# Optimization experiments

Measured on AMD Instinct MI355X. Metric: run time of the kernel, lower is better.

Reference implementation:

```python
import jax, jax.numpy as jnp
import numpy as np

# Model dims (match init_kwargs)
N_HEADS = 32
N_KV_HEADS = 8
DIM = 4096
HEAD_DIM = DIM // N_HEADS  # 128
N_REP = N_HEADS // N_KV_HEADS  # 4
MAX_SEQ_LEN = 2048
THETA = 10000.0


def precompute_freqs(dim, end, theta=THETA):
    inv = 1.0 / (theta ** (jnp.arange(0, dim, 2, dtype=jnp.float32) / dim))  # [dim/2]
    t = jnp.arange(end, dtype=jnp.float32)
    f = jnp.outer(t, inv)  # [end, dim/2]
    return jnp.cos(f), jnp.sin(f)


def apply_rope(x, cos, sin):
    # x: [b, s, h, d]; cos/sin: [s, d/2]. Pairs (x[...,2i], x[...,2i+1]) form complex numbers.
    xr = x[..., 0::2]
    xi = x[..., 1::2]
    c = cos[None, :, None, :]
    s = sin[None, :, None, :]
    out_r = xr * c - xi * s
    out_i = xr * s + xi * c
    return jnp.stack([out_r, out_i], axis=-1).reshape(x.shape)


def setup_inputs() -> dict:
    key = jax.random.key(0)
    ks = jax.random.split(key, 5)
    B, S = 4, 1024
    x = jax.random.normal(ks[0], (B, S, DIM), dtype=jnp.float32)
    wq = jax.random.normal(ks[1], (DIM, N_HEADS * HEAD_DIM), dtype=jnp.float32) * 0.02
    wk = jax.random.normal(ks[2], (DIM, N_KV_HEADS * HEAD_DIM), dtype=jnp.float32) * 0.02
    wv = jax.random.normal(ks[3], (DIM, N_KV_HEADS * HEAD_DIM), dtype=jnp.float32) * 0.02
    wo = jax.random.normal(ks[4], (N_HEADS * HEAD_DIM, DIM), dtype=jnp.float32) * 0.02
    # causal mask, additive: 0 on/below diagonal, -1e9 above
    mask = jnp.where(jnp.tril(jnp.ones((S, S), dtype=bool)), 0.0, -1e9).astype(jnp.float32)[None, None]
    return {"x": x, "wq": wq, "wk": wk, "wv": wv, "wo": wo, "mask": mask, "start_pos": 0}


def reference(x, wq, wk, wv, wo, mask, start_pos):
    B, S, _ = x.shape
    # QKV projections
    xq = (x @ wq).reshape(B, S, N_HEADS, HEAD_DIM)
    xk = (x @ wk).reshape(B, S, N_KV_HEADS, HEAD_DIM)
    xv = (x @ wv).reshape(B, S, N_KV_HEADS, HEAD_DIM)
    # RoPE on q, k at positions [start_pos, start_pos+S)
    cos, sin = precompute_freqs(HEAD_DIM, MAX_SEQ_LEN * 2)
    cos_s = jax.lax.dynamic_slice_in_dim(cos, start_pos, S, 0)
    sin_s = jax.lax.dynamic_slice_in_dim(sin, start_pos, S, 0)
    xq = apply_rope(xq, cos_s, sin_s)
    xk = apply_rope(xk, cos_s, sin_s)
    # KV-cache scatter-update (cache starts zeroed), then read prefix
    cache_k = jnp.zeros((B, MAX_SEQ_LEN, N_KV_HEADS, HEAD_DIM), dtype=x.dtype)
    cache_v = jnp.zeros_like(cache_k)
    cache_k = jax.lax.dynamic_update_slice(cache_k, xk, (0, start_pos, 0, 0))
    cache_v = jax.lax.dynamic_update_slice(cache_v, xv, (0, start_pos, 0, 0))
    kv_len = start_pos + S
    keys = cache_k[:, :kv_len]    # [b, kv_len, n_kv, d]
    values = cache_v[:, :kv_len]
    # GQA without materializing repeated KV: split q heads into (kv_group, rep)
    q = xq.reshape(B, S, N_KV_HEADS, N_REP, HEAD_DIM)
    scale = 1.0 / jnp.sqrt(jnp.float32(HEAD_DIM)).astype(x.dtype)
    scores = jnp.einsum('bsgrd,btgd->bgrst', q, keys) * scale  # [b, g, r, s, t]
    scores = scores + mask.reshape(1, 1, 1, S, kv_len)
    probs = jax.nn.softmax(scores, axis=-1)
    out = jnp.einsum('bgrst,btgd->bsgrd', probs, values)  # [b, s, g, r, d]
    out = out.reshape(B, S, N_HEADS * HEAD_DIM)
    return out @ wo
```

## Files before the change

kernel.cpp:

```cpp
#include <hip/hip_runtime.h>
#include <hip/hip_bf16.h>
#include <stdint.h>

typedef __bf16 bf16raw;
typedef __attribute__((ext_vector_type(8))) __bf16 bf16x8;
typedef __attribute__((ext_vector_type(4))) float f32x4;

#define DIMD 4096
#define NHEAD 32
#define NKVH 8
#define HD 128
#define SEQ 1024
#define NB 4
#define NTOK 4096
#define NQKV 6144

__device__ __forceinline__ void gload_lds16(const void* gsrc, void* ldst) {
  __builtin_amdgcn_global_load_lds(
      (const __attribute__((address_space(1))) void*)gsrc,
      (__attribute__((address_space(3))) void*)ldst, 16, 0, 0);
}

__global__ void cast_f32_bf16_kernel(const float* __restrict__ src,
                                     __hip_bfloat16* __restrict__ dst, int n) {
  int i = (blockIdx.x * 256 + threadIdx.x) * 8;
  if (i >= n) return;
  f32x4 a = *(const f32x4*)(src + i);
  f32x4 b = *(const f32x4*)(src + i + 4);
  union { bf16x8 v; __hip_bfloat16 e[8]; } o;
#pragma unroll
  for (int j = 0; j < 4; ++j) {
    o.e[j] = __float2bfloat16(a[j]);
    o.e[4 + j] = __float2bfloat16(b[j]);
  }
  *(bf16x8*)(dst + i) = o.v;
}

__global__ void transpose_qkv_kernel(const float* __restrict__ wq,
                                     const float* __restrict__ wk,
                                     const float* __restrict__ wv,
                                     __hip_bfloat16* __restrict__ dst) {
  __shared__ float tile[32][33];
  int n0 = blockIdx.x * 32;
  int k0 = blockIdx.y * 32;
  const float* src;
  int scol, nsw;
  if (n0 < 4096) { src = wq; scol = n0; nsw = 4096; }
  else if (n0 < 5120) { src = wk; scol = n0 - 4096; nsw = 1024; }
  else { src = wv; scol = n0 - 5120; nsw = 1024; }
  int tx = threadIdx.x, ty = threadIdx.y;
#pragma unroll
  for (int i = 0; i < 4; ++i)
    tile[ty + 8 * i][tx] = src[(size_t)(k0 + ty + 8 * i) * nsw + scol + tx];
  __syncthreads();
  union { ushort4 u; __hip_bfloat16 e[4]; } pk;
#pragma unroll
  for (int jj = 0; jj < 4; ++jj)
    pk.e[jj] = __float2bfloat16(tile[ty * 4 + jj][tx]);
  *(ushort4*)(dst + (size_t)(n0 + tx) * 4096 + k0 + ty * 4) = pk.u;
}

__global__ void transpose_wo_kernel(const float* __restrict__ src,
                                    __hip_bfloat16* __restrict__ dst) {
  __shared__ float tile[32][33];
  int n0 = blockIdx.x * 32, k0 = blockIdx.y * 32;
  int tx = threadIdx.x, ty = threadIdx.y;
#pragma unroll
  for (int i = 0; i < 4; ++i)
    tile[ty + 8 * i][tx] = src[(size_t)(k0 + ty + 8 * i) * 4096 + n0 + tx];
  __syncthreads();
  union { ushort4 u; __hip_bfloat16 e[4]; } pk;
#pragma unroll
  for (int jj = 0; jj < 4; ++jj)
    pk.e[jj] = __float2bfloat16(tile[ty * 4 + jj][tx]);
  *(ushort4*)(dst + (size_t)(n0 + tx) * 4096 + k0 + ty * 4) = pk.u;
}

__global__ void rope_table_kernel(float* __restrict__ cosb, float* __restrict__ sinb) {
  int idx = blockIdx.x * 256 + threadIdx.x;
  int s = idx >> 6, j = idx & 63;
  float inv = 1.0f / powf(10000.0f, (float)(2 * j) * (1.0f / 128.0f));
  float ang = (float)s * inv;
  cosb[idx] = cosf(ang);
  sinb[idx] = sinf(ang);
}


#define LGSB()                                       \
  asm volatile("s_waitcnt lgkmcnt(0)" ::: "memory"); \
  __builtin_amdgcn_sched_barrier(0)

#define QM_LO(AFR, MB)                                                     \
  _Pragma("unroll") for (int mf2 = 0; mf2 < 4; ++mf2)                      \
  _Pragma("unroll") for (int nf2 = 0; nf2 < 2; ++nf2)                      \
  _Pragma("unroll") for (int kk2 = 0; kk2 < 2; ++kk2)                      \
      acc[(MB) + mf2][nf2] = __builtin_amdgcn_mfma_f32_16x16x32_bf16(      \
          AFR[mf2 * 2 + kk2], bql[nf2 * 2 + kk2], acc[(MB) + mf2][nf2], 0, 0, 0)

#define QM_HI(AFR, MB)                                                     \
  _Pragma("unroll") for (int mf2 = 0; mf2 < 4; ++mf2)                      \
  _Pragma("unroll") for (int nf2 = 0; nf2 < NF - 2; ++nf2)                 \
  _Pragma("unroll") for (int kk2 = 0; kk2 < 2; ++kk2)                      \
      acc[(MB) + mf2][2 + nf2] = __builtin_amdgcn_mfma_f32_16x16x32_bf16(  \
          AFR[mf2 * 2 + kk2], bqh[nf2 * 2 + kk2], acc[(MB) + mf2][2 + nf2], 0, 0, 0)

#define TILE4(BUF, ST1, ST2, ST3, ST4, VM)                        \
  {                                                               \
    ST1;                                                          \
    _Pragma("unroll") for (int mf = 0; mf < 4; ++mf)              \
    _Pragma("unroll") for (int kk = 0; kk < 2; ++kk)              \
        alo[mf * 2 + kk] = ldsA(BUF, mf, kk);                     \
    _Pragma("unroll") for (int nf = 0; nf < 2; ++nf)              \
    _Pragma("unroll") for (int kk = 0; kk < 2; ++kk)              \
        bql[nf * 2 + kk] = ldsB(BUF, nf, kk);                     \
    LGSB();                                                       \
    __builtin_amdgcn_s_setprio(1);                                \
    QM_LO(alo, 0);                                                \
    __builtin_amdgcn_s_setprio(0);                                \
    _Pragma("unroll") for (int mf = 0; mf < 4; ++mf)              \
    _Pragma("unroll") for (int kk = 0; kk < 2; ++kk)              \
        ahi[mf * 2 + kk] = ldsA(BUF, mf + 4, kk);                 \
    ST2;                                                          \
    LGSB();                                                       \
    __builtin_amdgcn_s_setprio(1);                                \
    QM_LO(ahi, 4);                                                \
    __builtin_amdgcn_s_setprio(0);                                \
    _Pragma("unroll") for (int nf = 0; nf < NF - 2; ++nf)         \
    _Pragma("unroll") for (int kk = 0; kk < 2; ++kk)              \
        bqh[nf * 2 + kk] = ldsB(BUF, nf + 2, kk);                 \
    LGSB();                                                       \
    __builtin_amdgcn_s_setprio(1);                                \
    QM_HI(alo, 0);                                                \
    __builtin_amdgcn_s_setprio(0);                                \
    __builtin_amdgcn_s_barrier();   \
    ST3;                                                          \
    ST4;                                                          \
    __builtin_amdgcn_s_setprio(1);                                \
    QM_HI(ahi, 4);                                                \
    __builtin_amdgcn_s_setprio(0);                                \
    VM;                                                           \
    __builtin_amdgcn_s_barrier();   \
  }

template <typename OutT, bool ROPE, int BN, int XM, int XN, int PM, int PN>
__global__ __launch_bounds__(512, 2) void gemm256_kernel(
    const __hip_bfloat16* __restrict__ A, const __hip_bfloat16* __restrict__ BT,
    OutT* __restrict__ C, int M, int N, int K,
    const float* __restrict__ cosb, const float* __restrict__ sinb,
    __hip_bfloat16* __restrict__ vtc) {
  constexpr int NF = BN / 64;
  constexpr int BROWS_W = BN / 8;
  constexpr int BQ = BN / 4;
  constexpr int BUFS = 32768 + BN * 128;
  __shared__ __align__(16) char lds_[2 * BUFS];
  const int tid = threadIdx.x;
  const int w = tid >> 6, l = tid & 63;
  const int lr = l & 15, lk = l >> 4;
  const int wm = w >> 2, wn = w & 3;

  const int bid = blockIdx.x;
  const int x = bid & 7, idx = bid >> 3;
  const int xr = x % XM, xc = x / XM;
  const int m0 = (xr * PM + idx / PN) << 8;
  const int n0 = (xc * PN + idx % PN) * BN;

  const size_t Kb = (size_t)K * 2;
  const char* Ab = (const char*)A + (size_t)m0 * Kb;
  const char* Bb = (const char*)BT + (size_t)n0 * Kb;
  const int srcb = ((l & 7) ^ (l >> 3)) * 16;
  const int crow = l >> 3;

  auto stageA = [&](int buf, int half, int kt) {
#pragma unroll
    for (int j = 0; j < 2; ++j) {
      int row = half * 128 + (w * 2 + j) * 8 + crow;
      gload_lds16(Ab + (size_t)row * Kb + (size_t)kt * 128 + srcb,
                  lds_ + buf * BUFS + half * 16384 + (w * 2 + j) * 1024);
    }
  };
  auto stageBlo = [&](int buf, int kt) {
#pragma unroll
    for (int j = 0; j < 2; ++j) {
      int row = w * BROWS_W + j * 8 + crow;
      gload_lds16(Bb + (size_t)row * Kb + (size_t)kt * 128 + srcb,
                  lds_ + buf * BUFS + 32768 + (w * BROWS_W + j * 8) * 128);
    }
  };
  auto stageBhi = [&](int buf, int kt) {
#pragma unroll
    for (int j = 2; j < NF; ++j) {
      int row = w * BROWS_W + j * 8 + crow;
      gload_lds16(Bb + (size_t)row * Kb + (size_t)kt * 128 + srcb,
                  lds_ + buf * BUFS + 32768 + (w * BROWS_W + j * 8) * 128);
    }
  };
  auto ldsA = [&](int buf, int mf, int kk) {
    int rih = mf * 16 + lr;
    int cb = (kk * 64 + lk * 16) ^ ((lr & 7) << 4);
    return *(const bf16x8*)(lds_ + buf * BUFS + wm * 16384 + rih * 128 + cb);
  };
  auto ldsB = [&](int buf, int nf, int kk) {
    int row = wn * BQ + nf * 16 + lr;
    int cb = (kk * 64 + lk * 16) ^ ((lr & 7) << 4);
    return *(const bf16x8*)(lds_ + buf * BUFS + 32768 + row * 128 + cb);
  };

  f32x4 acc[8][NF] = {};
  bf16x8 alo[8], ahi[8], bql[4], bqh[4];

  stageA(0, 0, 0);
  stageA(0, 1, 0);
  stageBlo(0, 0);
  stageBhi(0, 0);
  stageA(1, 0, 1);
  stageA(1, 1, 1);
  asm volatile("s_waitcnt vmcnt(4)" ::: "memory");
  __builtin_amdgcn_s_barrier();

  const int NT = K >> 6;
  for (int E = 0; E < NT - 2; E += 2) {
    TILE4(0, stageBlo(1, E + 1), stageBhi(1, E + 1),
          stageA(0, 0, E + 2), stageA(0, 1, E + 2),
          asm volatile("s_waitcnt vmcnt(4)" ::: "memory"));
    TILE4(1, stageBlo(0, E + 2), stageBhi(0, E + 2),
          stageA(1, 0, E + 3), stageA(1, 1, E + 3),
          asm volatile("s_waitcnt vmcnt(4)" ::: "memory"));
  }
  TILE4(0, stageBlo(1, NT - 1), stageBhi(1, NT - 1), (void)0, (void)0,
        asm volatile("s_waitcnt vmcnt(0)" ::: "memory"));
  TILE4(1, (void)0, (void)0, (void)0, (void)0, (void)0);

#pragma unroll
  for (int mf = 0; mf < 8; ++mf) {
    int row = m0 + wm * 128 + mf * 16 + lk * 4;
#pragma unroll
    for (int nf = 0; nf < NF; ++nf) {
      int colb = n0 + wn * BQ + nf * 16;
      f32x4 v = acc[mf][nf];
      if constexpr (ROPE) {
        if (colb < 5120) {
          int d = (colb & 127) + lr;
          int jj = d >> 1;
          bool even = (d & 1) == 0;
#pragma unroll
          for (int j = 0; j < 4; ++j) {
            float p = __shfl_xor(v[j], 1);
            int s = (row + j) & (SEQ - 1);
            float c = cosb[s * 64 + jj];
            float sn = sinb[s * 64 + jj];
            v[j] = even ? (v[j] * c - p * sn) : (p * sn + v[j] * c);
          }
        } else {
          int col = colb + lr;
          int d = col & 127;
          int hk = (col >> 7) & 7;
          int b = row >> 10;
          int s = row & (SEQ - 1);
          union { uint64_t u; __hip_bfloat16 e[4]; } pk;
#pragma unroll
          for (int j = 0; j < 4; ++j) pk.e[j] = __float2bfloat16(v[j]);
          size_t off = ((size_t)((b * 8 + hk) * 16 + (s >> 6)) * 128 + d) * 64 +
                       (s & 63);
          *(uint64_t*)(vtc + off) = pk.u;
          continue;
        }
      }
#pragma unroll
      for (int j = 0; j < 4; ++j) {
        size_t off = (size_t)(row + j) * N + colb + lr;
        if constexpr (sizeof(OutT) == 2)
          C[off] = __float2bfloat16(v[j]);
        else
          C[off] = v[j];
      }
    }
  }
}

__global__ __launch_bounds__(512, 2) void attn_kernel(
    const __hip_bfloat16* __restrict__ qkv,
    const __hip_bfloat16* __restrict__ vtc,
    __hip_bfloat16* __restrict__ out) {
  __shared__ __align__(16) char Ks[2][16384];
  __shared__ __align__(16) char Vs[2][16384];
  __shared__ __align__(16) char Ps[8][4096];

  const int tid = threadIdx.x;
  const int w = tid >> 6, l = tid & 63;
  const int lr = l & 15, lk = l >> 4;
  const int bx = blockIdx.x;
  const int p = bx >> 5;
  const int bh = bx & 31;
  const int b = bh >> 3;
  const int hk = bh & 7;
  const int h = hk * 4 + (w & 3);
  const int qh = w >> 2;

  const char* KgB = (const char*)qkv +
                    ((size_t)(b * SEQ) * NQKV + DIMD + hk * HD) * 2;
  const char* VgB = (const char*)vtc + (size_t)(b * NKVH + hk) * (16 * 16384);
  char* Pw = &Ps[w][0];

  const float cs = 0.12752039889171495f;
  const float ebias = 11.541560327111707f;

  auto stageK = [&](int buf, int kvb) {
#pragma unroll
    for (int j = 0; j < 2; ++j) {
      int i2 = w * 2 + j;
      int row = i2 * 4 + (l >> 4);
      int si = ((l & 15) * 16) ^ ((row & 7) << 4);
      gload_lds16(KgB + (size_t)(kvb + row) * (NQKV * 2) + si,
                  &Ks[buf][i2 * 1024]);
    }
  };
  auto stageV = [&](int buf, int t) {
#pragma unroll
    for (int j = 0; j < 2; ++j) {
      int i2 = w * 2 + j;
      int row = i2 * 8 + (l >> 3);
      int si = ((l & 7) * 16) ^ ((row & 7) << 4);
      gload_lds16(VgB + (size_t)t * 16384 + row * 128 + si,
                  &Vs[buf][i2 * 1024]);
    }
  };

  for (int qsel = 0; qsel < 2; ++qsel) {
    const int qtile = qsel ? (15 - p) : p;
    const int qbaseW = qtile * 64 + qh * 32;
    const int nkv = qtile + 1;

    bf16x8 aq[8];
#pragma unroll
    for (int qg = 0; qg < 2; ++qg) {
      const __hip_bfloat16* Qp =
          qkv + (size_t)(b * SEQ + qbaseW + qg * 16 + lr) * NQKV + h * HD + lk * 8;
#pragma unroll
      for (int ks = 0; ks < 4; ++ks) aq[qg * 4 + ks] = *(const bf16x8*)(Qp + ks * 32);
    }

    f32x4 O[16] = {};
    float lsum[8] = {0.f, 0.f, 0.f, 0.f, 0.f, 0.f, 0.f, 0.f};

    stageK(0, 0);
    stageV(0, 0);
    asm volatile("s_waitcnt vmcnt(0)" ::: "memory");
    __syncthreads();

    for (int t = 0; t < nkv; ++t) {
      const int cur = t & 1;
      if (t + 1 < nkv) {
        stageK(cur ^ 1, (t + 1) * 64);
        stageV(cur ^ 1, t + 1);
      }
      const int kvb = t * 64;

      f32x4 st[8] = {};
      __builtin_amdgcn_s_setprio(1);
#pragma unroll
      for (int nt = 0; nt < 4; ++nt) {
        int row = nt * 16 + lr;
        const char* kr = &Ks[cur][row * 256];
        int sw = (row & 7) << 4;
        bf16x8 bk[4];
#pragma unroll
        for (int ks = 0; ks < 4; ++ks)
          bk[ks] = *(const bf16x8*)(kr + ((ks * 64 + lk * 16) ^ sw));
#pragma unroll
        for (int qg = 0; qg < 2; ++qg)
#pragma unroll
          for (int ks = 0; ks < 4; ++ks)
            st[qg * 4 + nt] = __builtin_amdgcn_mfma_f32_16x16x32_bf16(
                aq[qg * 4 + ks], bk[ks], st[qg * 4 + nt], 0, 0, 0);
      }
      __builtin_amdgcn_s_setprio(0);

#pragma unroll
      for (int qg = 0; qg < 2; ++qg) {
        const bool needmask = (kvb + 63 > qbaseW + qg * 16);
#pragma unroll
        for (int j = 0; j < 4; ++j) {
          int qrow = qbaseW + qg * 16 + lk * 4 + j;
          int prow = lk * 4 + j;
          int sw = (prow & 7) << 4;
#pragma unroll
          for (int nt = 0; nt < 4; ++nt) {
            float pv = exp2f(fmaf(st[qg * 4 + nt][j], cs, -ebias));
            if (needmask && (kvb + nt * 16 + lr > qrow)) pv = 0.f;
            lsum[qg * 4 + j] += pv;
            *(__hip_bfloat16*)(Pw + qg * 2048 + prow * 128 +
                               (((nt * 16 + lr) * 2) ^ sw)) = __float2bfloat16(pv);
          }
        }
      }

      asm volatile("s_waitcnt lgkmcnt(0)" ::: "memory");
      __builtin_amdgcn_sched_barrier(0);

      __builtin_amdgcn_s_setprio(1);
#pragma unroll
      for (int ks = 0; ks < 2; ++ks) {
        bf16x8 ap[2];
#pragma unroll
        for (int qg = 0; qg < 2; ++qg)
          ap[qg] = *(const bf16x8*)(Pw + qg * 2048 + lr * 128 +
                                    ((ks * 64 + lk * 16) ^ ((lr & 7) << 4)));
#pragma unroll
        for (int dt = 0; dt < 8; ++dt) {
          int row = dt * 16 + lr;
          bf16x8 bv = *(const bf16x8*)(&Vs[cur][row * 128 +
                                               ((ks * 64 + lk * 16) ^ ((row & 7) << 4))]);
#pragma unroll
          for (int qg = 0; qg < 2; ++qg)
            O[qg * 8 + dt] = __builtin_amdgcn_mfma_f32_16x16x32_bf16(
                ap[qg], bv, O[qg * 8 + dt], 0, 0, 0);
        }
      }
      __builtin_amdgcn_s_setprio(0);

      __syncthreads();
    }

#pragma unroll
    for (int qg = 0; qg < 2; ++qg) {
#pragma unroll
      for (int j = 0; j < 4; ++j) {
        float rs = lsum[qg * 4 + j];
        rs += __shfl_xor(rs, 1);
        rs += __shfl_xor(rs, 2);
        rs += __shfl_xor(rs, 4);
        rs += __shfl_xor(rs, 8);
        float inv = 1.0f / rs;
        __hip_bfloat16* orow =
            out + (size_t)(b * SEQ + qbaseW + qg * 16 + lk * 4 + j) * DIMD + h * HD;
#pragma unroll
        for (int dt = 0; dt < 8; ++dt)
          orow[dt * 16 + lr] = __float2bfloat16(O[qg * 8 + dt][j] * inv);
      }
    }
  }
}

extern "C" void kernel_launch(void* const* d_in, const int* in_sizes, int n_in,
                              void* d_out, int out_size, void* d_ws, size_t ws_size,
                              hipStream_t stream) {
  const float* x = (const float*)d_in[0];
  const float* wq = (const float*)d_in[1];
  const float* wk = (const float*)d_in[2];
  const float* wv = (const float*)d_in[3];
  const float* wo = (const float*)d_in[4];
  float* out = (float*)d_out;

  char* ws = (char*)d_ws;
  const size_t MB = 1024 * 1024;
  __hip_bfloat16* xb = (__hip_bfloat16*)(ws);
  __hip_bfloat16* wqkvt = (__hip_bfloat16*)(ws + 32 * MB);
  __hip_bfloat16* wot = (__hip_bfloat16*)(ws + 80 * MB);
  __hip_bfloat16* qkv = (__hip_bfloat16*)(ws + 112 * MB);
  __hip_bfloat16* vtc = (__hip_bfloat16*)(ws + 160 * MB);
  float* cosb = (float*)(ws + 168 * MB);
  float* sinb = cosb + SEQ * 64;

  cast_f32_bf16_kernel<<<NTOK * DIMD / 8 / 256, 256, 0, stream>>>(x, xb, NTOK * DIMD);
  transpose_qkv_kernel<<<dim3(192, 128), dim3(32, 8), 0, stream>>>(wq, wk, wv, wqkvt);
  transpose_wo_kernel<<<dim3(128, 128), dim3(32, 8), 0, stream>>>(wo, wot);
  rope_table_kernel<<<SEQ * 64 / 256, 256, 0, stream>>>(cosb, sinb);
  gemm256_kernel<__hip_bfloat16, true, 192, 2, 4, 8, 8><<<dim3(512), 512, 0, stream>>>(
      xb, wqkvt, qkv, NTOK, NQKV, DIMD, cosb, sinb, vtc);
  attn_kernel<<<dim3(256), 512, 0, stream>>>(qkv, vtc, xb);
  gemm256_kernel<float, false, 256, 4, 2, 4, 8><<<dim3(256), 512, 0, stream>>>(
      xb, wot, out, NTOK, DIMD, DIMD, nullptr, nullptr, nullptr);
}
```

Measured before the change: 444.2 us.

## Halve attention query tile per block and double grid for higher occupancy

The attention kernel now gives each warp one 16-row query group instead of two, so each block covers 32 query rows and the grid doubles to 512 blocks. Causal load balancing still pairs tile p with tile 31-p. Accumulator and P-buffer sizes halve, and the launch bounds ask for 4 blocks per CU instead of 2, to improve occupancy and latency hiding. In exchange, each K/V tile staged in LDS is reused by half as many query rows, which roughly doubles K/V load traffic.

After: 443.5 us. Within noise of the previous version (-0.1%).

```diff
diff --git a/kernel.cpp b/kernel.cpp
--- a/kernel.cpp
+++ b/kernel.cpp
@@ -277,13 +277,13 @@
   }
 }
 
-__global__ __launch_bounds__(512, 2) void attn_kernel(
+__global__ __launch_bounds__(512, 4) void attn_kernel(
     const __hip_bfloat16* __restrict__ qkv,
     const __hip_bfloat16* __restrict__ vtc,
     __hip_bfloat16* __restrict__ out) {
   __shared__ __align__(16) char Ks[2][16384];
   __shared__ __align__(16) char Vs[2][16384];
-  __shared__ __align__(16) char Ps[8][4096];
+  __shared__ __align__(16) char Ps[8][2048];
 
   const int tid = threadIdx.x;
   const int w = tid >> 6, l = tid & 63;
@@ -326,21 +326,20 @@
   };
 
   for (int qsel = 0; qsel < 2; ++qsel) {
-    const int qtile = qsel ? (15 - p) : p;
-    const int qbaseW = qtile * 64 + qh * 32;
-    const int nkv = qtile + 1;
-
-    bf16x8 aq[8];
-#pragma unroll
-    for (int qg = 0; qg < 2; ++qg) {
+    const int qtile = qsel ? (31 - p) : p;
+    const int qbase = qtile * 32 + qh * 16;
+    const int nkv = (qtile >> 1) + 1;
+
+    bf16x8 aq[4];
+    {
       const __hip_bfloat16* Qp =
-          qkv + (size_t)(b * SEQ + qbaseW + qg * 16 + lr) * NQKV + h * HD + lk * 8;
-#pragma unroll
-      for (int ks = 0; ks < 4; ++ks) aq[qg * 4 + ks] = *(const bf16x8*)(Qp + ks * 32);
-    }
-
-    f32x4 O[16] = {};
-    float lsum[8] = {0.f, 0.f, 0.f, 0.f, 0.f, 0.f, 0.f, 0.f};
+          qkv + (size_t)(b * SEQ + qbase + lr) * NQKV + h * HD + lk * 8;
+#pragma unroll
+      for (int ks = 0; ks < 4; ++ks) aq[ks] = *(const bf16x8*)(Qp + ks * 32);
+    }
+
+    f32x4 O[8] = {};
+    float lsum[4] = {0.f, 0.f, 0.f, 0.f};
 
     stageK(0, 0);
     stageV(0, 0);
@@ -355,42 +354,34 @@
       }
       const int kvb = t * 64;
 
-      f32x4 st[8] = {};
+      f32x4 st[4] = {};
       __builtin_amdgcn_s_setprio(1);
 #pragma unroll
       for (int nt = 0; nt < 4; ++nt) {
         int row = nt * 16 + lr;
         const char* kr = &Ks[cur][row * 256];
         int sw = (row & 7) << 4;
-        bf16x8 bk[4];
-#pragma unroll
-        for (int ks = 0; ks < 4; ++ks)
-          bk[ks] = *(const bf16x8*)(kr + ((ks * 64 + lk * 16) ^ sw));
-#pragma unroll
-        for (int qg = 0; qg < 2; ++qg)
-#pragma unroll
-          for (int ks = 0; ks < 4; ++ks)
-            st[qg * 4 + nt] = __builtin_amdgcn_mfma_f32_16x16x32_bf16(
-                aq[qg * 4 + ks], bk[ks], st[qg * 4 + nt], 0, 0, 0);
+#pragma unroll
+        for (int ks = 0; ks < 4; ++ks) {
+          bf16x8 bk = *(const bf16x8*)(kr + ((ks * 64 + lk * 16) ^ sw));
+          st[nt] = __builtin_amdgcn_mfma_f32_16x16x32_bf16(aq[ks], bk, st[nt], 0, 0, 0);
+        }
       }
       __builtin_amdgcn_s_setprio(0);
 
-#pragma unroll
-      for (int qg = 0; qg < 2; ++qg) {
-        const bool needmask = (kvb + 63 > qbaseW + qg * 16);
-#pragma unroll
-        for (int j = 0; j < 4; ++j) {
-          int qrow = qbaseW + qg * 16 + lk * 4 + j;
-          int prow = lk * 4 + j;
-          int sw = (prow & 7) << 4;
-#pragma unroll
-          for (int nt = 0; nt < 4; ++nt) {
-            float pv = exp2f(fmaf(st[qg * 4 + nt][j], cs, -ebias));
-            if (needmask && (kvb + nt * 16 + lr > qrow)) pv = 0.f;
-            lsum[qg * 4 + j] += pv;
-            *(__hip_bfloat16*)(Pw + qg * 2048 + prow * 128 +
-                               (((nt * 16 + lr) * 2) ^ sw)) = __float2bfloat16(pv);
-          }
+      const bool needmask = (kvb + 63 > qbase);
+#pragma unroll
+      for (int j = 0; j < 4; ++j) {
+        int qrow = qbase + lk * 4 + j;
+        int prow = lk * 4 + j;
+        int sw = (prow & 7) << 4;
+#pragma unroll
+        for (int nt = 0; nt < 4; ++nt) {
+          float pv = exp2f(fmaf(st[nt][j], cs, -ebias));
+          if (needmask && (kvb + nt * 16 + lr > qrow)) pv = 0.f;
+          lsum[j] += pv;
+          *(__hip_bfloat16*)(Pw + prow * 128 + (((nt * 16 + lr) * 2) ^ sw)) =
+              __float2bfloat16(pv);
         }
       }
 
@@ -400,20 +391,14 @@
       __builtin_amdgcn_s_setprio(1);
 #pragma unroll
       for (int ks = 0; ks < 2; ++ks) {
-        bf16x8 ap[2];
-#pragma unroll
-        for (int qg = 0; qg < 2; ++qg)
-          ap[qg] = *(const bf16x8*)(Pw + qg * 2048 + lr * 128 +
-                                    ((ks * 64 + lk * 16) ^ ((lr & 7) << 4)));
+        bf16x8 ap = *(const bf16x8*)(Pw + lr * 128 +
+                                     ((ks * 64 + lk * 16) ^ ((lr & 7) << 4)));
 #pragma unroll
         for (int dt = 0; dt < 8; ++dt) {
           int row = dt * 16 + lr;
           bf16x8 bv = *(const bf16x8*)(&Vs[cur][row * 128 +
                                                ((ks * 64 + lk * 16) ^ ((row & 7) << 4))]);
-#pragma unroll
-          for (int qg = 0; qg < 2; ++qg)
-            O[qg * 8 + dt] = __builtin_amdgcn_mfma_f32_16x16x32_bf16(
-                ap[qg], bv, O[qg * 8 + dt], 0, 0, 0);
+          O[dt] = __builtin_amdgcn_mfma_f32_16x16x32_bf16(ap, bv, O[dt], 0, 0, 0);
         }
       }
       __builtin_amdgcn_s_setprio(0);
@@ -422,21 +407,18 @@
     }
 
 #pragma unroll
-    for (int qg = 0; qg < 2; ++qg) {
-#pragma unroll
-      for (int j = 0; j < 4; ++j) {
-        float rs = lsum[qg * 4 + j];
-        rs += __shfl_xor(rs, 1);
-        rs += __shfl_xor(rs, 2);
-        rs += __shfl_xor(rs, 4);
-        rs += __shfl_xor(rs, 8);
-        float inv = 1.0f / rs;
-        __hip_bfloat16* orow =
-            out + (size_t)(b * SEQ + qbaseW + qg * 16 + lk * 4 + j) * DIMD + h * HD;
-#pragma unroll
-        for (int dt = 0; dt < 8; ++dt)
-          orow[dt * 16 + lr] = __float2bfloat16(O[qg * 8 + dt][j] * inv);
-      }
+    for (int j = 0; j < 4; ++j) {
+      float rs = lsum[j];
+      rs += __shfl_xor(rs, 1);
+      rs += __shfl_xor(rs, 2);
+      rs += __shfl_xor(rs, 4);
+      rs += __shfl_xor(rs, 8);
+      float inv = 1.0f / rs;
+      __hip_bfloat16* orow =
+          out + (size_t)(b * SEQ + qbase + lk * 4 + j) * DIMD + h * HD;
+#pragma unroll
+      for (int dt = 0; dt < 8; ++dt)
+        orow[dt * 16 + lr] = __float2bfloat16(O[dt][j] * inv);
     }
   }
 }
@@ -467,7 +449,7 @@
   rope_table_kernel<<<SEQ * 64 / 256, 256, 0, stream>>>(cosb, sinb);
   gemm256_kernel<__hip_bfloat16, true, 192, 2, 4, 8, 8><<<dim3(512), 512, 0, stream>>>(
       xb, wqkvt, qkv, NTOK, NQKV, DIMD, cosb, sinb, vtc);
-  attn_kernel<<<dim3(256), 512, 0, stream>>>(qkv, vtc, xb);
+  attn_kernel<<<dim3(512), 512, 0, stream>>>(qkv, vtc, xb);
   gemm256_kernel<float, false, 256, 4, 2, 4, 8><<<dim3(256), 512, 0, stream>>>(
       xb, wot, out, NTOK, DIMD, DIMD, nullptr, nullptr, nullptr);
 }
```
